# Optimization experiments

Measured on AMD Instinct MI355X. Metric: run time of the kernel, lower is better.

## Reference

```python
import jax, jax.numpy as jnp
import numpy as np
import math

QUERY_DIM = 512
FEAT_DIM = 2048
HID_DIM = 512
OUT_DIM = 512
B, L, S, T = 32, 128, 36, 36


def _linear_params(key, d_in, d_out):
    kw, kb = jax.random.split(key)
    scale = 1.0 / math.sqrt(d_in)
    W = jax.random.uniform(kw, (d_in, d_out), jnp.float32, -scale, scale)
    b = jax.random.uniform(kb, (d_out,), jnp.float32, -scale, scale)
    return W, b


def setup_inputs() -> dict:
    key = jax.random.key(0)
    ks = jax.random.split(key, 9)
    query = jax.random.normal(ks[0], (B, L, QUERY_DIM), jnp.float32)
    src = jax.random.normal(ks[1], (B, S, FEAT_DIM), jnp.float32)
    trg = jax.random.normal(ks[2], (B, T, FEAT_DIM), jnp.float32)
    Wq, bq = _linear_params(ks[3], QUERY_DIM, HID_DIM)
    Ws, bs = _linear_params(ks[4], FEAT_DIM, HID_DIM)
    Wt, bt = _linear_params(ks[5], FEAT_DIM, HID_DIM)
    Wsv, bsv = _linear_params(ks[6], FEAT_DIM, HID_DIM)
    Wtv, btv = _linear_params(ks[7], FEAT_DIM, HID_DIM)
    Wo, bo = _linear_params(ks[8], HID_DIM * 2 + QUERY_DIM, OUT_DIM)
    return dict(query=query, src=src, trg=trg,
                Wq=Wq, bq=bq, Ws=Ws, bs=bs, Wt=Wt, bt=bt,
                Wsv=Wsv, bsv=bsv, Wtv=Wtv, btv=btv, Wo=Wo, bo=bo)


def reference(query, src, trg, Wq, bq, Ws, bs, Wt, bt, Wsv, bsv, Wtv, btv, Wo, bo):
    b, l, _ = query.shape
    s = src.shape[1]
    t = trg.shape[1]
    q = query @ Wq + bq                      # (b, l, h)
    s_key = src @ Ws + bs                    # (b, s, h)
    t_key = trg @ Wt + bt                    # (b, t, h)
    # Faithful to torch: s_key.unsqueeze(1) + t_key.unsqueeze(2) -> (b, t, s, h),
    # then labeled 'istk' in the einsum (requires s == t).
    rel_key = (s_key[:, None, :, :] + t_key[:, :, None, :]) * 0.5  # (b, t, s, h)
    weight = jnp.einsum('blk,bstk->blst', q, rel_key) / math.sqrt(HID_DIM)
    weight = jax.nn.softmax(weight.reshape(b, l, s * t), axis=-1).reshape(b, l, s, t)
    s_value = src @ Wsv + bsv                # (b, s, h)
    t_value = trg @ Wtv + btv                # (b, t, h)
    s_ctx = jnp.einsum('blst,bsh->blh', weight, s_value)
    t_ctx = jnp.einsum('blst,bth->blh', weight, t_value)
    x = jnp.concatenate((query, s_ctx, t_ctx), axis=-1)
    return jax.nn.relu(x @ Wo + bo)
```

## Files before the change

kernel.cpp:

```cpp
#include <hip/hip_runtime.h>
#include <hip/hip_bf16.h>
#include <math.h>

#define DEVI __device__ __forceinline__

typedef __attribute__((ext_vector_type(4))) float f32x4;
typedef __attribute__((ext_vector_type(8))) short bf16x8;

DEVI unsigned short f2bf(float f) {
  union { float f; unsigned int u; } v; v.f = f;
  return (unsigned short)((v.u + 0x7FFFu + ((v.u >> 16) & 1u)) >> 16);
}
DEVI float bf2f(unsigned short s) {
  union { unsigned int u; float f; } v; v.u = ((unsigned int)s) << 16; return v.f;
}
DEVI bf16x8 pack8(f32x4 a, f32x4 b) {
  bf16x8 r;
  r[0] = (short)f2bf(a[0]); r[1] = (short)f2bf(a[1]);
  r[2] = (short)f2bf(a[2]); r[3] = (short)f2bf(a[3]);
  r[4] = (short)f2bf(b[0]); r[5] = (short)f2bf(b[1]);
  r[6] = (short)f2bf(b[2]); r[7] = (short)f2bf(b[3]);
  return r;
}
DEVI void gload16(const unsigned short* g, unsigned short* l) {
  __builtin_amdgcn_global_load_lds(
      (const __attribute__((address_space(1))) unsigned int*)g,
      (__attribute__((address_space(3))) unsigned int*)l, 16, 0, 0);
}
#define SBAR() do { asm volatile("" ::: "memory"); \
                    __builtin_amdgcn_s_barrier();  \
                    asm volatile("" ::: "memory"); } while (0)

struct PrepJobs {
  const float* src[9];
  unsigned short* dst[9];
  int K[9];
  int base[9];
  int type[9];
};

__global__ __launch_bounds__(256) void prep(PrepJobs J) {
  __shared__ float t[64][65];
  int tile = blockIdx.x;
  int job = 0;
  while (job < 8 && tile >= J.base[job + 1]) ++job;
  int tl = tile - J.base[job];
  int K = J.K[job];
  if (J.type[job] == 0) {
    int tn = tl & 7, tk = tl >> 3;
    int x = threadIdx.x & 63, y = threadIdx.x >> 6;
    const float* s = J.src[job];
    int k0 = tk * 64, n0 = tn * 64;
#pragma unroll
    for (int yy = y; yy < 64; yy += 4)
      t[yy][x] = s[(size_t)(k0 + yy) * 512 + n0 + x];
    __syncthreads();
    unsigned short* d = J.dst[job];
    int kb = (x >> 3) & 7, ko = x & 7;
#pragma unroll
    for (int yy = y; yy < 64; yy += 4) {
      int n = n0 + yy;
      int kswz = k0 + (((kb + n) & 7) << 3) + ko;
      d[(size_t)n * K + kswz] = f2bf(t[x][yy]);
    }
  } else {
    int nk = K >> 6;
    int rt = tl / nk;
    int r0 = rt * 64, k0 = (tl - rt * nk) * 64;
    int r = threadIdx.x >> 2, kq = threadIdx.x & 3;
    int row = r0 + r;
    const float* s = J.src[job] + (size_t)row * K + k0 + kq * 16;
    f32x4 a0 = *(const f32x4*)s;
    f32x4 a1 = *(const f32x4*)(s + 4);
    f32x4 a2 = *(const f32x4*)(s + 8);
    f32x4 a3 = *(const f32x4*)(s + 12);
    unsigned short* d = J.dst[job] + (size_t)row * K + k0;
    int kb0 = kq * 2;
    *(bf16x8*)(d + ((kb0 + row) & 7) * 8) = pack8(a0, a1);
    *(bf16x8*)(d + ((kb0 + 1 + row) & 7) * 8) = pack8(a2, a3);
  }
}

struct GJob {
  const unsigned short* A0;
  const unsigned short* Bt;
  const float* bias;
  unsigned short* Cb;
  int Astride, Bstride, Cstride, nTilesN, nt, mode, tileBase;
};
struct GBatch { GJob j[7]; int njobs; int swz; };

template <int MI, int NI>
__global__ __launch_bounds__(256) void gemm_pipe(GBatch batch) {
  constexpr int BM = MI * 32, BN = NI * 32;
  int gt = blockIdx.x;
  if (batch.swz) {
    int cpx = gridDim.x >> 3;
    gt = (blockIdx.x & 7) * cpx + (blockIdx.x >> 3);
  }
  int job = 0;
#pragma unroll
  for (int i = 1; i < 7; ++i)
    if (i < batch.njobs && gt >= batch.j[i].tileBase) job = i;
  GJob J = batch.j[job];
  int tl = gt - J.tileBase;
  int bm = (tl / J.nTilesN) * BM, bn = (tl % J.nTilesN) * BN;

  __shared__ __align__(16) unsigned short La[2][BM * 64];
  __shared__ __align__(16) unsigned short Lb[2][BN * 64];

  int tid = threadIdx.x;
  int wave = tid >> 6, lane = tid & 63;
  int lrow = lane & 15, lq = lane >> 4;
  int wr = (wave >> 1) * (MI * 16), wc = (wave & 1) * (NI * 16);
  f32x4 acc[MI][NI] = {};

  int nt = J.nt;

  auto stage_both = [&](int t, int buf) {
    const unsigned short* GA = J.A0 + (size_t)bm * J.Astride + (size_t)(t << 6);
    const unsigned short* GB = J.Bt + (size_t)bn * J.Bstride + (size_t)(t << 6);
#pragma unroll
    for (int p = 0; p < MI; ++p) {
      int s = p * 256 + tid;
      gload16(GA + (size_t)(s >> 3) * J.Astride + (s & 7) * 8,
              &La[buf][(size_t)(p * 256 + wave * 64) * 8]);
    }
#pragma unroll
    for (int p = 0; p < NI; ++p) {
      int s = p * 256 + tid;
      gload16(GB + (size_t)(s >> 3) * J.Bstride + (s & 7) * 8,
              &Lb[buf][(size_t)(p * 256 + wave * 64) * 8]);
    }
  };

  stage_both(0, 0);
  if (nt > 1) stage_both(1, 1);

  for (int t = 0; t < nt; ++t) {
    if (t + 1 < nt) {
      if constexpr (MI + NI == 8)      asm volatile("s_waitcnt vmcnt(8)" ::: "memory");
      else if constexpr (MI + NI == 6) asm volatile("s_waitcnt vmcnt(6)" ::: "memory");
      else                             asm volatile("s_waitcnt vmcnt(4)" ::: "memory");
    } else {
      asm volatile("s_waitcnt vmcnt(0)" ::: "memory");
    }
    SBAR();
    int cur = t & 1;
#pragma unroll
    for (int kc = 0; kc < 2; ++kc) {
      int kb = kc * 4 + lq;
      bf16x8 af[MI], bv[NI];
#pragma unroll
      for (int mi = 0; mi < MI; ++mi) {
        int r = wr + mi * 16 + lrow;
        af[mi] = *(const bf16x8*)&La[cur][r * 64 + ((kb + r) & 7) * 8];
      }
#pragma unroll
      for (int ni = 0; ni < NI; ++ni) {
        int r = wc + ni * 16 + lrow;
        bv[ni] = *(const bf16x8*)&Lb[cur][r * 64 + ((kb + r) & 7) * 8];
      }
#pragma unroll
      for (int mi = 0; mi < MI; ++mi)
#pragma unroll
        for (int ni = 0; ni < NI; ++ni)
          acc[mi][ni] = __builtin_amdgcn_mfma_f32_16x16x32_bf16(af[mi], bv[ni], acc[mi][ni], 0, 0, 0);
    }
    SBAR();
    if (t + 2 < nt) stage_both(t + 2, cur);
  }

#pragma unroll
  for (int mi = 0; mi < MI; ++mi) {
#pragma unroll
    for (int ni = 0; ni < NI; ++ni) {
      int gn = bn + wc + ni * 16 + lrow;
      float bvs = J.bias ? J.bias[gn] : 0.f;
      int gm0 = bm + wr + mi * 16 + lq * 4;
      if (J.mode == 0) {
#pragma unroll
        for (int r = 0; r < 4; ++r)
          J.Cb[(size_t)(gm0 + r) * J.Cstride + gn] = f2bf(acc[mi][ni][r] + bvs);
      } else {
#pragma unroll
        for (int r = 0; r < 4; ++r) {
          int row = gm0 + r;
          int col = (gn & ~63) | (((((gn >> 3) & 7) + row) & 7) << 3) | (gn & 7);
          J.Cb[(size_t)row * J.Cstride + col] = f2bf(acc[mi][ni][r] + bvs);
        }
      }
    }
  }
}

struct HJob {
  const unsigned short* A0;
  const unsigned short* Bt;
  unsigned short* Cb;
  int Astride, Bstride, Cstride, nTilesN, nt, tileBase;
};
struct S3Args {
  HJob g[2];
  int nGemm;
  const unsigned short* qh;
  const unsigned short* s_key;
  const unsigned short* t_key;
  float* Wsw;
  float* Wtw;
};

__global__ __launch_bounds__(256) void stage3(S3Args A) {
  __shared__ __align__(16) unsigned char smem[16384];
  int tid = threadIdx.x;
  int wave = tid >> 6, lane = tid & 63;
  int lrow = lane & 15, lq = lane >> 4;

  if ((int)blockIdx.x < A.nGemm) {
    unsigned short* Ls = (unsigned short*)smem;
    int gt = blockIdx.x;
    HJob J = (gt >= A.g[1].tileBase) ? A.g[1] : A.g[0];
    int tl = gt - J.tileBase;
    int bm = (tl / J.nTilesN) * 64, bn = (tl % J.nTilesN) * 64;
    int wr = (wave >> 1) * 32, wc = (wave & 1) * 32;
    f32x4 acc[2][2] = {};
    int nt = J.nt;

    auto stage_both = [&](int t, int buf) {
      const unsigned short* GA = J.A0 + (size_t)bm * J.Astride + (size_t)(t << 6);
      const unsigned short* GB = J.Bt + (size_t)bn * J.Bstride + (size_t)(t << 6);
#pragma unroll
      for (int p = 0; p < 2; ++p) {
        int s = p * 256 + tid;
        gload16(GA + (size_t)(s >> 3) * J.Astride + (s & 7) * 8,
                &Ls[(size_t)buf * 2048 + (size_t)((p * 256 + wave * 64) & 1023) * 8
                    + (size_t)(p >> 1) * 0]);
      }
#pragma unroll
      for (int p = 0; p < 2; ++p) {
        int s = p * 256 + tid;
        gload16(GB + (size_t)(s >> 3) * J.Bstride + (s & 7) * 8,
                &Ls[4096 + (size_t)buf * 2048 + (size_t)(p * 256 + wave * 64) * 8]);
      }
    };
    (void)stage_both;

    unsigned short* La0 = (unsigned short*)smem;
    unsigned short* Lb0 = La0 + 2 * 4096;
    __shared__ __align__(16) unsigned short Lg[2][4096 + 4096];
    auto stage2 = [&](int t, int buf) {
      const unsigned short* GA = J.A0 + (size_t)bm * J.Astride + (size_t)(t << 6);
      const unsigned short* GB = J.Bt + (size_t)bn * J.Bstride + (size_t)(t << 6);
#pragma unroll
      for (int p = 0; p < 2; ++p) {
        int s = p * 256 + tid;
        gload16(GA + (size_t)(s >> 3) * J.Astride + (s & 7) * 8,
                &Lg[buf][(size_t)(p * 256 + wave * 64) * 8]);
      }
#pragma unroll
      for (int p = 0; p < 2; ++p) {
        int s = p * 256 + tid;
        gload16(GB + (size_t)(s >> 3) * J.Bstride + (s & 7) * 8,
                &Lg[buf][4096 + (size_t)(p * 256 + wave * 64) * 8]);
      }
    };

    stage2(0, 0);
    if (nt > 1) stage2(1, 1);

    for (int t = 0; t < nt; ++t) {
      if (t + 1 < nt) asm volatile("s_waitcnt vmcnt(4)" ::: "memory");
      else            asm volatile("s_waitcnt vmcnt(0)" ::: "memory");
      SBAR();
      int cur = t & 1;
#pragma unroll
      for (int kc = 0; kc < 2; ++kc) {
        int kb = kc * 4 + lq;
        bf16x8 af[2], bv[2];
#pragma unroll
        for (int mi = 0; mi < 2; ++mi) {
          int r = wr + mi * 16 + lrow;
          af[mi] = *(const bf16x8*)&Lg[cur][r * 64 + ((kb + r) & 7) * 8];
        }
#pragma unroll
        for (int ni = 0; ni < 2; ++ni) {
          int r = wc + ni * 16 + lrow;
          bv[ni] = *(const bf16x8*)&Lg[cur][4096 + r * 64 + ((kb + r) & 7) * 8];
        }
#pragma unroll
        for (int mi = 0; mi < 2; ++mi)
#pragma unroll
          for (int ni = 0; ni < 2; ++ni)
            acc[mi][ni] = __builtin_amdgcn_mfma_f32_16x16x32_bf16(af[mi], bv[ni], acc[mi][ni], 0, 0, 0);
      }
      SBAR();
      if (t + 2 < nt) stage2(t + 2, cur);
    }
#pragma unroll
    for (int mi = 0; mi < 2; ++mi) {
#pragma unroll
      for (int ni = 0; ni < 2; ++ni) {
        int gn = bn + wc + ni * 16 + lrow;
        int gm0 = bm + wr + mi * 16 + lq * 4;
#pragma unroll
        for (int r = 0; r < 4; ++r)
          J.Cb[(size_t)(gm0 + r) * J.Cstride + gn] = f2bf(acc[mi][ni][r]);
      }
    }
  } else {
    float (*red)[3][64][4] = (float(*)[3][64][4])smem;
    int bid2 = blockIdx.x - A.nGemm;
    int b = bid2 >> 3, lc = bid2 & 7;
    int mat = wave >> 1, kh = wave & 1;
    int row0 = b * 128 + lc * 16;
    const unsigned short* qp = A.qh + (size_t)row0 * 512;
    const unsigned short* key = (mat ? A.s_key : A.t_key) + (size_t)b * 36 * 512;
    f32x4 acc[3] = {};
    for (int kc = kh * 8; kc < kh * 8 + 8; ++kc) {
      int k = kc * 32 + lq * 8;
      bf16x8 af = *(const bf16x8*)(qp + (size_t)lrow * 512 + k);
#pragma unroll
      for (int nf = 0; nf < 3; ++nf) {
        int n = nf * 16 + lrow; if (n > 35) n = 35;
        bf16x8 bv = *(const bf16x8*)(key + (size_t)n * 512 + k);
        acc[nf] = __builtin_amdgcn_mfma_f32_16x16x32_bf16(af, bv, acc[nf], 0, 0, 0);
      }
    }
#pragma unroll
    for (int nf = 0; nf < 3; ++nf)
      *(f32x4*)&red[wave][nf][lane][0] = acc[nf];
    __syncthreads();

    if (kh == 0) {
      const float ccs = 0.022097086912079608f;
      float ex[3][4];
#pragma unroll
      for (int r = 0; r < 4; ++r) {
        float a0 = (red[wave][0][lane][r] + red[wave + 1][0][lane][r]) * ccs;
        float a1 = (red[wave][1][lane][r] + red[wave + 1][1][lane][r]) * ccs;
        float a2 = (lrow < 4)
            ? (red[wave][2][lane][r] + red[wave + 1][2][lane][r]) * ccs : -1e30f;
        float mx = fmaxf(fmaxf(a0, a1), a2);
        for (int s = 1; s < 16; s <<= 1) mx = fmaxf(mx, __shfl_xor(mx, s));
        float e0 = __expf(a0 - mx), e1 = __expf(a1 - mx);
        float e2 = (lrow < 4) ? __expf(a2 - mx) : 0.f;
        float sum = e0 + e1 + e2;
        for (int s = 1; s < 16; s <<= 1) sum += __shfl_xor(sum, s);
        float inv = 1.f / sum;
        ex[0][r] = e0 * inv; ex[1][r] = e1 * inv; ex[2][r] = e2 * inv;
      }
      float* W = mat ? A.Wtw : A.Wsw;
#pragma unroll
      for (int nf = 0; nf < 3; ++nf) {
        int col = nf * 16 + lrow;
        if (col < 36) {
#pragma unroll
          for (int r = 0; r < 4; ++r)
            W[(size_t)(row0 + lq * 4 + r) * 36 + col] = ex[nf][r];
        }
      }
    }
  }
}

__global__ __launch_bounds__(256) void wsum(
    const float* __restrict__ Wsw, const float* __restrict__ Wtw,
    const unsigned short* __restrict__ svp, const unsigned short* __restrict__ tvp,
    const unsigned short* __restrict__ Pb, float* __restrict__ out) {
  __shared__ float wlT[2][36][16];
  int b = blockIdx.x, lc = blockIdx.y;
  int tid = threadIdx.x;
  int row0 = b * 128 + lc * 16;
  for (int i = tid; i < 2 * 16 * 36; i += 256) {
    int m = i / 576, rem = i - m * 576;
    int l = rem / 36, j = rem - l * 36;
    wlT[m][j][l] = (m ? Wtw : Wsw)[(size_t)(row0 + l) * 36 + j];
  }
  __syncthreads();

  int lgrp = tid >> 6, hgrp = tid & 63;
  float a2[4][8] = {};
#pragma unroll
  for (int m = 0; m < 2; ++m) {
    const unsigned short* V = (m ? tvp : svp) + (size_t)b * 36 * 512;
    for (int j = 0; j < 36; ++j) {
      f32x4 wa = *(const f32x4*)&wlT[m][j][lgrp * 4];
      bf16x8 v = *(const bf16x8*)(V + (size_t)j * 512 + hgrp * 8);
      float vf[8];
#pragma unroll
      for (int hi = 0; hi < 8; ++hi) vf[hi] = bf2f((unsigned short)v[hi]);
#pragma unroll
      for (int li = 0; li < 4; ++li)
#pragma unroll
        for (int hi = 0; hi < 8; ++hi) a2[li][hi] += wa[li] * vf[hi];
    }
  }
#pragma unroll
  for (int li = 0; li < 4; ++li) {
    int R = row0 + lgrp * 4 + li;
    bf16x8 p = *(const bf16x8*)(Pb + (size_t)R * 512 + hgrp * 8);
    float* op = out + (size_t)R * 512 + hgrp * 8;
    f32x4 o0, o1;
#pragma unroll
    for (int hi = 0; hi < 4; ++hi) {
      o0[hi] = fmaxf(bf2f((unsigned short)p[hi]) + a2[li][hi], 0.f);
      o1[hi] = fmaxf(bf2f((unsigned short)p[4 + hi]) + a2[li][4 + hi], 0.f);
    }
    *(f32x4*)op = o0;
    *(f32x4*)(op + 4) = o1;
  }
}

extern "C" void kernel_launch(void* const* d_in, const int* in_sizes, int n_in,
                              void* d_out, int out_size, void* d_ws, size_t ws_size,
                              hipStream_t stream) {
  (void)in_sizes; (void)n_in; (void)out_size; (void)ws_size;
  const float* query = (const float*)d_in[0];
  const float* src   = (const float*)d_in[1];
  const float* trg   = (const float*)d_in[2];
  const float* Wq  = (const float*)d_in[3];  const float* bq  = (const float*)d_in[4];
  const float* Wsk = (const float*)d_in[5];  const float* bs  = (const float*)d_in[6];
  const float* Wtk = (const float*)d_in[7];  const float* bt  = (const float*)d_in[8];
  const float* Wsv = (const float*)d_in[9];  const float* bsv = (const float*)d_in[10];
  const float* Wtv = (const float*)d_in[11]; const float* btv = (const float*)d_in[12];
  const float* Wo  = (const float*)d_in[13]; const float* bo  = (const float*)d_in[14];

  unsigned short* WqT    = (unsigned short*)d_ws;
  unsigned short* WsT    = WqT  + 512 * 512;
  unsigned short* WtT    = WsT  + 512 * 2048;
  unsigned short* WsvT   = WtT  + 512 * 2048;
  unsigned short* WtvT   = WsvT + 512 * 2048;
  unsigned short* WoT    = WtvT + 512 * 2048;
  unsigned short* queryB = WoT  + 512 * 1536;
  unsigned short* srcB   = queryB + 4096 * 512;
  unsigned short* trgB   = srcB + 1152 * 2048;
  unsigned short* qh     = trgB + 1152 * 2048;
  unsigned short* s_key  = qh + 4096 * 512;
  unsigned short* t_key  = s_key + 1152 * 512;
  unsigned short* s_val  = t_key + 1152 * 512;
  unsigned short* t_val  = s_val + 1152 * 512;
  unsigned short* svp    = t_val + 1152 * 512;
  unsigned short* tvp    = svp + 1152 * 512;
  unsigned short* Pb     = tvp + 1152 * 512;
  float* Wsw = (float*)(Pb + 4096 * 512);
  float* Wtw = Wsw + 4096 * 36;
  float* out = (float*)d_out;

  PrepJobs pj;
  const float* psrc[9] = { Wq, Wsk, Wtk, Wsv, Wtv, Wo, query, src, trg };
  unsigned short* pdst[9] = { WqT, WsT, WtT, WsvT, WtvT, WoT, queryB, srcB, trgB };
  int pK[9]    = { 512, 2048, 2048, 2048, 2048, 1536, 512, 2048, 2048 };
  int ptype[9] = { 0, 0, 0, 0, 0, 0, 1, 1, 1 };
  int prows[9] = { 0, 0, 0, 0, 0, 0, 4096, 1152, 1152 };
  int pbase = 0;
  for (int i = 0; i < 9; ++i) {
    pj.src[i] = psrc[i]; pj.dst[i] = pdst[i]; pj.K[i] = pK[i]; pj.type[i] = ptype[i];
    pj.base[i] = pbase;
    pbase += ptype[i] ? (prows[i] / 64) * (pK[i] / 64) : (pK[i] / 64) * 8;
  }
  prep<<<pbase, 256, 0, stream>>>(pj);

  {
    GBatch pb;
    pb.swz = 0;
    int base = 0;
    const unsigned short* Aarr[4] = { srcB, trgB, srcB, trgB };
    const unsigned short* Barr[4] = { WsT, WtT, WsvT, WtvT };
    const float* biasArr[4] = { bs, bt, bsv, btv };
    unsigned short* Carr[4] = { s_key, t_key, s_val, t_val };
    for (int i = 0; i < 4; ++i) {
      GJob& j = pb.j[i];
      j.A0 = Aarr[i]; j.Bt = Barr[i]; j.bias = biasArr[i]; j.Cb = Carr[i];
      j.Astride = 2048; j.Bstride = 2048; j.Cstride = 512;
      j.nTilesN = 4; j.nt = 32; j.mode = (i < 2) ? 0 : 2;
      j.tileBase = base; base += 18 * 4;
    }
    {
      GJob& j = pb.j[4];
      j.A0 = queryB; j.Bt = WqT; j.bias = bq; j.Cb = qh;
      j.Astride = 512; j.Bstride = 512; j.Cstride = 512;
      j.nTilesN = 4; j.nt = 8; j.mode = 0;
      j.tileBase = base; base += 64 * 4;
    }
    {
      GJob& j = pb.j[5];
      j.A0 = queryB; j.Bt = WoT; j.bias = bo; j.Cb = Pb;
      j.Astride = 512; j.Bstride = 1536; j.Cstride = 512;
      j.nTilesN = 4; j.nt = 8; j.mode = 0;
      j.tileBase = base; base += 64 * 4;
    }
    pb.j[6] = pb.j[5]; pb.j[6].tileBase = 0x7fffffff;
    pb.njobs = 6;
    gemm_pipe<2, 4><<<base, 256, 0, stream>>>(pb);
  }

  {
    S3Args sa;
    HJob& a = sa.g[0];
    a.A0 = s_val; a.Bt = WoT + 512; a.Cb = svp;
    a.Astride = 512; a.Bstride = 1536; a.Cstride = 512;
    a.nTilesN = 8; a.nt = 8; a.tileBase = 0;
    HJob& b2 = sa.g[1];
    b2 = a;
    b2.A0 = t_val; b2.Bt = WoT + 1024; b2.Cb = tvp;
    b2.tileBase = 18 * 8;
    sa.nGemm = 288;
    sa.qh = qh; sa.s_key = s_key; sa.t_key = t_key;
    sa.Wsw = Wsw; sa.Wtw = Wtw;
    stage3<<<288 + 256, 256, 0, stream>>>(sa);
  }

  wsum<<<dim3(32, 8), 256, 0, stream>>>(Wsw, Wtw, svp, tvp, Pb, out);
}
```

Baseline: 73.11 us.

## Split wsum over hidden halves, add MFMA priority hints, merge stage3 LDS buffers

Result: no change. 73.23 us (+0.2%).

```diff
diff --git a/kernel.cpp b/kernel.cpp
--- a/kernel.cpp
+++ b/kernel.cpp
@@ -147,6 +147,7 @@
     }
     SBAR();
     int cur = t & 1;
+    __builtin_amdgcn_s_setprio(1);
 #pragma unroll
     for (int kc = 0; kc < 2; ++kc) {
       int kb = kc * 4 + lq;
@@ -167,6 +168,7 @@
         for (int ni = 0; ni < NI; ++ni)
           acc[mi][ni] = __builtin_amdgcn_mfma_f32_16x16x32_bf16(af[mi], bv[ni], acc[mi][ni], 0, 0, 0);
     }
+    __builtin_amdgcn_s_setprio(0);
     SBAR();
     if (t + 2 < nt) stage_both(t + 2, cur);
   }
@@ -211,13 +213,12 @@
 };
 
 __global__ __launch_bounds__(256) void stage3(S3Args A) {
-  __shared__ __align__(16) unsigned char smem[16384];
+  __shared__ __align__(16) unsigned short SH[2][8192];
   int tid = threadIdx.x;
   int wave = tid >> 6, lane = tid & 63;
   int lrow = lane & 15, lq = lane >> 4;
 
   if ((int)blockIdx.x < A.nGemm) {
-    unsigned short* Ls = (unsigned short*)smem;
     int gt = blockIdx.x;
     HJob J = (gt >= A.g[1].tileBase) ? A.g[1] : A.g[0];
     int tl = gt - J.tileBase;
@@ -226,42 +227,20 @@
     f32x4 acc[2][2] = {};
     int nt = J.nt;
 
-    auto stage_both = [&](int t, int buf) {
+    auto stage2 = [&](int t, int buf) {
       const unsigned short* GA = J.A0 + (size_t)bm * J.Astride + (size_t)(t << 6);
       const unsigned short* GB = J.Bt + (size_t)bn * J.Bstride + (size_t)(t << 6);
 #pragma unroll
       for (int p = 0; p < 2; ++p) {
         int s = p * 256 + tid;
         gload16(GA + (size_t)(s >> 3) * J.Astride + (s & 7) * 8,
-                &Ls[(size_t)buf * 2048 + (size_t)((p * 256 + wave * 64) & 1023) * 8
-                    + (size_t)(p >> 1) * 0]);
+                &SH[buf][(size_t)(p * 256 + wave * 64) * 8]);
       }
 #pragma unroll
       for (int p = 0; p < 2; ++p) {
         int s = p * 256 + tid;
         gload16(GB + (size_t)(s >> 3) * J.Bstride + (s & 7) * 8,
-                &Ls[4096 + (size_t)buf * 2048 + (size_t)(p * 256 + wave * 64) * 8]);
-      }
-    };
-    (void)stage_both;
-
-    unsigned short* La0 = (unsigned short*)smem;
-    unsigned short* Lb0 = La0 + 2 * 4096;
-    __shared__ __align__(16) unsigned short Lg[2][4096 + 4096];
-    auto stage2 = [&](int t, int buf) {
-      const unsigned short* GA = J.A0 + (size_t)bm * J.Astride + (size_t)(t << 6);
-      const unsigned short* GB = J.Bt + (size_t)bn * J.Bstride + (size_t)(t << 6);
-#pragma unroll
-      for (int p = 0; p < 2; ++p) {
-        int s = p * 256 + tid;
-        gload16(GA + (size_t)(s >> 3) * J.Astride + (s & 7) * 8,
-                &Lg[buf][(size_t)(p * 256 + wave * 64) * 8]);
-      }
-#pragma unroll
-      for (int p = 0; p < 2; ++p) {
-        int s = p * 256 + tid;
-        gload16(GB + (size_t)(s >> 3) * J.Bstride + (s & 7) * 8,
-                &Lg[buf][4096 + (size_t)(p * 256 + wave * 64) * 8]);
+                &SH[buf][4096 + (size_t)(p * 256 + wave * 64) * 8]);
       }
     };
 
@@ -273,6 +252,7 @@
       else            asm volatile("s_waitcnt vmcnt(0)" ::: "memory");
       SBAR();
       int cur = t & 1;
+      __builtin_amdgcn_s_setprio(1);
 #pragma unroll
       for (int kc = 0; kc < 2; ++kc) {
         int kb = kc * 4 + lq;
@@ -280,12 +260,12 @@
 #pragma unroll
         for (int mi = 0; mi < 2; ++mi) {
           int r = wr + mi * 16 + lrow;
-          af[mi] = *(const bf16x8*)&Lg[cur][r * 64 + ((kb + r) & 7) * 8];
+          af[mi] = *(const bf16x8*)&SH[cur][r * 64 + ((kb + r) & 7) * 8];
         }
 #pragma unroll
         for (int ni = 0; ni < 2; ++ni) {
           int r = wc + ni * 16 + lrow;
-          bv[ni] = *(const bf16x8*)&Lg[cur][4096 + r * 64 + ((kb + r) & 7) * 8];
+          bv[ni] = *(const bf16x8*)&SH[cur][4096 + r * 64 + ((kb + r) & 7) * 8];
         }
 #pragma unroll
         for (int mi = 0; mi < 2; ++mi)
@@ -293,6 +273,7 @@
           for (int ni = 0; ni < 2; ++ni)
             acc[mi][ni] = __builtin_amdgcn_mfma_f32_16x16x32_bf16(af[mi], bv[ni], acc[mi][ni], 0, 0, 0);
       }
+      __builtin_amdgcn_s_setprio(0);
       SBAR();
       if (t + 2 < nt) stage2(t + 2, cur);
     }
@@ -308,7 +289,7 @@
       }
     }
   } else {
-    float (*red)[3][64][4] = (float(*)[3][64][4])smem;
+    float (*red)[3][64][4] = (float(*)[3][64][4])&SH[0][0];
     int bid2 = blockIdx.x - A.nGemm;
     int b = bid2 >> 3, lc = bid2 & 7;
     int mat = wave >> 1, kh = wave & 1;
@@ -369,6 +350,7 @@
     const unsigned short* __restrict__ Pb, float* __restrict__ out) {
   __shared__ float wlT[2][36][16];
   int b = blockIdx.x, lc = blockIdx.y;
+  int h0 = blockIdx.z << 8;
   int tid = threadIdx.x;
   int row0 = b * 128 + lc * 16;
   for (int i = tid; i < 2 * 16 * 36; i += 256) {
@@ -378,28 +360,31 @@
   }
   __syncthreads();
 
-  int lgrp = tid >> 6, hgrp = tid & 63;
-  float a2[4][8] = {};
+  int lgrp = tid >> 5;
+  int hgrp = tid & 31;
+  float a2[2][8] = {};
 #pragma unroll
   for (int m = 0; m < 2; ++m) {
-    const unsigned short* V = (m ? tvp : svp) + (size_t)b * 36 * 512;
+    const unsigned short* V = (m ? tvp : svp) + (size_t)b * 36 * 512 + h0;
     for (int j = 0; j < 36; ++j) {
-      f32x4 wa = *(const f32x4*)&wlT[m][j][lgrp * 4];
+      float w0 = wlT[m][j][lgrp * 2];
+      float w1 = wlT[m][j][lgrp * 2 + 1];
       bf16x8 v = *(const bf16x8*)(V + (size_t)j * 512 + hgrp * 8);
       float vf[8];
 #pragma unroll
       for (int hi = 0; hi < 8; ++hi) vf[hi] = bf2f((unsigned short)v[hi]);
 #pragma unroll
-      for (int li = 0; li < 4; ++li)
-#pragma unroll
-        for (int hi = 0; hi < 8; ++hi) a2[li][hi] += wa[li] * vf[hi];
-    }
-  }
-#pragma unroll
-  for (int li = 0; li < 4; ++li) {
-    int R = row0 + lgrp * 4 + li;
-    bf16x8 p = *(const bf16x8*)(Pb + (size_t)R * 512 + hgrp * 8);
-    float* op = out + (size_t)R * 512 + hgrp * 8;
+      for (int hi = 0; hi < 8; ++hi) {
+        a2[0][hi] += w0 * vf[hi];
+        a2[1][hi] += w1 * vf[hi];
+      }
+    }
+  }
+#pragma unroll
+  for (int li = 0; li < 2; ++li) {
+    int R = row0 + lgrp * 2 + li;
+    bf16x8 p = *(const bf16x8*)(Pb + (size_t)R * 512 + h0 + hgrp * 8);
+    float* op = out + (size_t)R * 512 + h0 + hgrp * 8;
     f32x4 o0, o1;
 #pragma unroll
     for (int hi = 0; hi < 4; ++hi) {
@@ -510,5 +495,5 @@
     stage3<<<288 + 256, 256, 0, stream>>>(sa);
   }
 
-  wsum<<<dim3(32, 8), 256, 0, stream>>>(Wsw, Wtw, svp, tvp, Pb, out);
-}
+  wsum<<<dim3(32, 8, 2), 256, 0, stream>>>(Wsw, Wtw, svp, tvp, Pb, out);
+}
```
